# Kernel optimization log

Measured on AMD Instinct MI355X. Metric: run time of the kernel, lower is better.

## Reference

```python
import jax, jax.numpy as jnp
import numpy as np

TEMPERATURE = 30.0
LN_EPS = 1e-5

B, CIN, COUT, S, HID, K = 64, 256, 512, 4096, 64, 4


def setup_inputs() -> dict:
    key = jax.random.key(0)
    ks = jax.random.split(key, 4)
    x = jax.random.normal(ks[0], (B, CIN, S), dtype=jnp.float32)
    w1 = jax.random.normal(ks[1], (HID, CIN), dtype=jnp.float32) * (1.0 / np.sqrt(CIN))
    w2 = jax.random.normal(ks[2], (K, HID), dtype=jnp.float32) * (1.0 / np.sqrt(HID))
    b2 = jnp.zeros((K,), dtype=jnp.float32)
    conv_w = jax.random.normal(ks[3], (K, COUT, CIN), dtype=jnp.float32) * (1.0 / np.sqrt(CIN))
    conv_b = jnp.zeros((K, COUT), dtype=jnp.float32)
    gamma = jnp.ones((S,), dtype=jnp.float32)
    beta = jnp.zeros((S,), dtype=jnp.float32)
    return {"x": x, "w1": w1, "w2": w2, "b2": b2, "conv_w": conv_w,
            "conv_b": conv_b, "gamma": gamma, "beta": beta}


def reference(x, w1, w2, b2, conv_w, conv_b, gamma, beta):
    # --- attention over K kernel experts (global avg pool -> FC -> ReLU -> FC -> softmax/T) ---
    pooled = x.mean(axis=-1)                               # [B, Cin]
    h = jax.nn.relu(pooled @ w1.T)                         # [B, H]
    logits = h @ w2.T + b2                                 # [B, K]
    att = jax.nn.softmax(logits / TEMPERATURE, axis=-1)    # [B, K]
    # --- per-sample mixed 1x1 conv weights (grouped-conv trick == batched matmul) ---
    Wb = jnp.einsum('bk,koi->boi', att, conv_w)            # [B, Cout, Cin]
    bb = att @ conv_b                                      # [B, Cout]
    y = jnp.einsum('boi,bis->bos', Wb, x) + bb[:, :, None]  # [B, Cout, S]
    # --- LayerNorm over time axis (Samples) ---
    mu = y.mean(axis=-1, keepdims=True)
    var = y.var(axis=-1, keepdims=True)
    y = (y - mu) * jax.lax.rsqrt(var + LN_EPS) * gamma + beta
    # --- GELU (torch default: exact erf); dropout is identity in eval mode ---
    return jax.nn.gelu(y, approximate=False)
```

## Files before the change

### kernel.cpp

```cpp
#include <hip/hip_runtime.h>
#include <hip/hip_bf16.h>

#define B_   64
#define CIN  256
#define COUT 512
#define S_   4096
#define HID  64
#define KEXP 4

typedef float f32x4 __attribute__((ext_vector_type(4)));
typedef short bf16x8 __attribute__((ext_vector_type(8)));

static __device__ __forceinline__ unsigned short f2bf(float f) {
    union { float f; unsigned u; } c; c.f = f;
    unsigned r = c.u + 0x7FFFu + ((c.u >> 16) & 1u);
    return (unsigned short)(r >> 16);
}
static __device__ __forceinline__ float bf2f(unsigned short u) {
    union { unsigned u; float f; } c; c.u = ((unsigned)u) << 16;
    return c.f;
}

#define GSTR 68
__global__ __launch_bounds__(512, 2) void k_gram_part(const float* __restrict__ x,
                                                      float* __restrict__ part,
                                                      float* __restrict__ ppart,
                                                      unsigned short* __restrict__ xF) {
    __shared__ unsigned short lds[256 * GSTR];
    int bid = blockIdx.x;
    int b = bid & 63, sc = bid >> 6;
    int t = threadIdx.x, lane = t & 63, wv = t >> 6;
    int wr = wv >> 1, wc = wv & 1;
    const float* xb = x + (size_t)b * CIN * S_;
    unsigned short* xFb = xF + (size_t)b * S_ * CIN;

    f32x4 acc[4][8] = {};
    float psum[8] = {0.f, 0.f, 0.f, 0.f, 0.f, 0.f, 0.f, 0.f};

    for (int step = 0; step < 16; ++step) {
        int s0 = sc * 1024 + step * 64;
        __syncthreads();
#pragma unroll
        for (int p = 0; p < 8; ++p) {
            int i = t + p * 512;
            int row = i >> 4, f4 = i & 15;
            float4 v = *(const float4*)(xb + (size_t)row * S_ + s0 + f4 * 4);
            psum[p] += v.x + v.y + v.z + v.w;
            unsigned short u[4] = {f2bf(v.x), f2bf(v.y), f2bf(v.z), f2bf(v.w)};
            *(uint2*)&lds[row * GSTR + f4 * 4] = *(const uint2*)u;
        }
        __syncthreads();
        {
#pragma unroll
            for (int it = 0; it < 4; ++it) {
                int slot = t + it * 512;
                int chunk = slot >> 6;
                int st_l = chunk >> 3, kb = chunk & 7;
                int l = slot & 63;
                unsigned short tmp[8];
#pragma unroll
                for (int j = 0; j < 8; ++j)
                    tmp[j] = lds[(kb * 32 + (l >> 4) * 8 + j) * GSTR + st_l * 16 + (l & 15)];
                *(uint4*)(xFb + ((size_t)((s0 >> 4) + st_l) * 8 + kb) * 512 + l * 8) = *(const uint4*)tmp;
            }
        }
#pragma unroll
        for (int kk = 0; kk < 2; ++kk) {
            bf16x8 bfr[8];
#pragma unroll
            for (int nf = 0; nf < 8; ++nf)
                bfr[nf] = *(const bf16x8*)&lds[(wc * 128 + nf * 16 + (lane & 15)) * GSTR + kk * 32 + (lane >> 4) * 8];
#pragma unroll
            for (int mfi = 0; mfi < 4; ++mfi) {
                bf16x8 afr = *(const bf16x8*)&lds[(wr * 64 + mfi * 16 + (lane & 15)) * GSTR + kk * 32 + (lane >> 4) * 8];
#pragma unroll
                for (int nf = 0; nf < 8; ++nf)
                    acc[mfi][nf] = __builtin_amdgcn_mfma_f32_16x16x32_bf16(afr, bfr[nf], acc[mfi][nf], 0, 0, 0);
            }
        }
    }
#pragma unroll
    for (int p = 0; p < 8; ++p) {
        float s = psum[p];
        s += __shfl_xor(s, 1); s += __shfl_xor(s, 2);
        s += __shfl_xor(s, 4); s += __shfl_xor(s, 8);
        if ((t & 15) == 0) ppart[((size_t)sc * 64 + b) * 256 + ((t + p * 512) >> 4)] = s;
    }
    float* pb = part + ((size_t)sc * 64 + b) * 65536;
#pragma unroll
    for (int mfi = 0; mfi < 4; ++mfi) {
#pragma unroll
        for (int r = 0; r < 4; ++r) {
            int row = wr * 64 + mfi * 16 + (lane >> 4) * 4 + r;
#pragma unroll
            for (int nf = 0; nf < 8; ++nf)
                pb[row * 256 + wc * 128 + nf * 16 + (lane & 15)] = acc[mfi][nf][r];
        }
    }
}

__global__ __launch_bounds__(256) void k_gred(const float* __restrict__ part,
                                              const float* __restrict__ ppart,
                                              unsigned short* __restrict__ ghat,
                                              float* __restrict__ pooled) {
    int b = blockIdx.x, t = threadIdx.x;
    const size_t bo = (size_t)b * 65536;
    const size_t scs = (size_t)64 * 65536;
    const float inv = 1.f / S_;
    for (int it = 0; it < 64; ++it) {
        size_t i = (size_t)(it * 256 + t) * 4;
        float4 a0 = *(const float4*)(part + bo + i);
        float4 a1 = *(const float4*)(part + scs + bo + i);
        float4 a2 = *(const float4*)(part + 2 * scs + bo + i);
        float4 a3 = *(const float4*)(part + 3 * scs + bo + i);
        unsigned short u[4] = {f2bf((a0.x + a1.x + a2.x + a3.x) * inv),
                               f2bf((a0.y + a1.y + a2.y + a3.y) * inv),
                               f2bf((a0.z + a1.z + a2.z + a3.z) * inv),
                               f2bf((a0.w + a1.w + a2.w + a3.w) * inv)};
        *(uint2*)&ghat[bo + i] = *(const uint2*)u;
    }
    float p = ppart[(size_t)b * 256 + t] + ppart[(size_t)(64 + b) * 256 + t]
            + ppart[(size_t)(128 + b) * 256 + t] + ppart[(size_t)(192 + b) * 256 + t];
    pooled[b * 256 + t] = p * inv;
}

__global__ __launch_bounds__(64) void k_att(const float* __restrict__ pooled,
                                            const float* __restrict__ w1,
                                            const float* __restrict__ w2,
                                            const float* __restrict__ b2,
                                            float* __restrict__ att_out) {
    int b = blockIdx.x, t = threadIdx.x;
    __shared__ float pl[CIN];
    __shared__ float hl[HID];
    __shared__ float satt[KEXP];
    for (int j = t; j < CIN; j += 64) pl[j] = pooled[b * CIN + j];
    __syncthreads();
    float acc = 0.f;
    const float* w1r = w1 + t * CIN;
#pragma unroll 4
    for (int c = 0; c < CIN; c += 4) {
        float4 w = *(const float4*)(w1r + c);
        acc += w.x * pl[c] + w.y * pl[c + 1] + w.z * pl[c + 2] + w.w * pl[c + 3];
    }
    hl[t] = fmaxf(acc, 0.f);
    __syncthreads();
    if (t < KEXP) {
        float a = 0.f;
        for (int j = 0; j < HID; ++j) a += hl[j] * w2[t * HID + j];
        satt[t] = (a + b2[t]) * (1.0f / 30.0f);
    }
    __syncthreads();
    if (t == 0) {
        float m = fmaxf(fmaxf(satt[0], satt[1]), fmaxf(satt[2], satt[3]));
        float e0 = expf(satt[0] - m), e1 = expf(satt[1] - m);
        float e2 = expf(satt[2] - m), e3 = expf(satt[3] - m);
        float inv = 1.f / (e0 + e1 + e2 + e3);
        att_out[b * KEXP + 0] = e0 * inv;
        att_out[b * KEXP + 1] = e1 * inv;
        att_out[b * KEXP + 2] = e2 * inv;
        att_out[b * KEXP + 3] = e3 * inv;
    }
}

__global__ __launch_bounds__(256) void k_wb(const float* __restrict__ conv_w,
                                            const float* __restrict__ att,
                                            unsigned short* __restrict__ wb) {
    int bid = blockIdx.x;
    int b = bid >> 5, o0 = (bid & 31) * 16;
    int t = threadIdx.x;
    int o = o0 + (t >> 4);
    int i0 = (t & 15) * 16;
    float ak[KEXP];
#pragma unroll
    for (int k = 0; k < KEXP; ++k) ak[k] = att[b * KEXP + k];
    float acc[16];
#pragma unroll
    for (int j = 0; j < 16; ++j) acc[j] = 0.f;
#pragma unroll
    for (int k = 0; k < KEXP; ++k) {
        const float* src = conv_w + ((size_t)(k * COUT + o)) * CIN + i0;
#pragma unroll
        for (int j4 = 0; j4 < 4; ++j4) {
            float4 v = *(const float4*)(src + j4 * 4);
            acc[j4 * 4 + 0] += ak[k] * v.x;
            acc[j4 * 4 + 1] += ak[k] * v.y;
            acc[j4 * 4 + 2] += ak[k] * v.z;
            acc[j4 * 4 + 3] += ak[k] * v.w;
        }
    }
    unsigned short us[16];
#pragma unroll
    for (int j = 0; j < 16; ++j) us[j] = f2bf(acc[j]);
    unsigned short* dst = wb + (size_t)(b * COUT + o) * CIN + i0;
    *(uint4*)(dst) = *(const uint4*)(us);
    *(uint4*)(dst + 8) = *(const uint4*)(us + 8);
}

#define ASTR 264

__global__ __launch_bounds__(256, 2) void k_z(const unsigned short* __restrict__ wb,
                                              const unsigned short* __restrict__ ghat,
                                              float* __restrict__ zout) {
    __shared__ unsigned short lds_a[128 * ASTR];
    int bid = blockIdx.x;
    int b = bid & 63;
    int tile = bid >> 6;
    int m0 = (tile & 3) * 128, n0 = (tile >> 2) * 128;
    int t = threadIdx.x;
    {
        int row = t >> 1, half = t & 1;
        const unsigned short* src = wb + (size_t)(b * COUT + m0 + row) * CIN + half * 128;
        unsigned short* dstrow = &lds_a[row * ASTR + half * 128];
#pragma unroll
        for (int j = 0; j < 16; ++j)
            *(uint4*)(dstrow + j * 8) = *(const uint4*)(src + j * 8);
    }
    __syncthreads();

    int lane = t & 63;
    int wid = t >> 6;
    int arow = lane & 15;
    int kq = lane >> 4;
    int col0 = n0 + wid * 32 + (lane & 15);
    int col1 = col0 + 16;
    const unsigned short* gb = ghat + (size_t)b * 256 * 256;

    f32x4 acc[8][2] = {};
#pragma unroll
    for (int kk = 0; kk < 8; ++kk) {
        bf16x8 b0 = *(const bf16x8*)(gb + (size_t)col0 * 256 + kk * 32 + kq * 8);
        bf16x8 b1 = *(const bf16x8*)(gb + (size_t)col1 * 256 + kk * 32 + kq * 8);
#pragma unroll
        for (int mf = 0; mf < 8; ++mf) {
            int row = mf * 16 + arow;
            bf16x8 a = *(const bf16x8*)&lds_a[row * ASTR + kk * 32 + kq * 8];
            acc[mf][0] = __builtin_amdgcn_mfma_f32_16x16x32_bf16(a, b0, acc[mf][0], 0, 0, 0);
            acc[mf][1] = __builtin_amdgcn_mfma_f32_16x16x32_bf16(a, b1, acc[mf][1], 0, 0, 0);
        }
    }
#pragma unroll
    for (int mf = 0; mf < 8; ++mf) {
#pragma unroll
        for (int r = 0; r < 4; ++r) {
            int row = m0 + mf * 16 + (lane >> 4) * 4 + r;
            size_t rb = ((size_t)b * COUT + row) * 256;
#pragma unroll
            for (int nf = 0; nf < 2; ++nf) {
                int col = n0 + wid * 32 + nf * 16 + (lane & 15);
                zout[rb + col] = acc[mf][nf][r];
            }
        }
    }
}

__global__ __launch_bounds__(256) void k_v(const float* __restrict__ z,
                                           const unsigned short* __restrict__ wb,
                                           const float* __restrict__ pooled,
                                           float* __restrict__ mu,
                                           float* __restrict__ rstd) {
    int gid = blockIdx.x * 4 + (threadIdx.x >> 6);
    int lane = threadIdx.x & 63;
    int b = gid >> 9;
    const float* zr = z + (size_t)gid * 256;
    const unsigned short* wr = wb + (size_t)gid * 256;

    float4 zv = *(const float4*)(zr + lane * 4);
    ushort4 wu = *(const ushort4*)(wr + lane * 4);
    float w0 = bf2f(wu.x), w1 = bf2f(wu.y), w2 = bf2f(wu.z), w3 = bf2f(wu.w);
    float4 pv = *(const float4*)(pooled + b * CIN + lane * 4);

    float v = zv.x * w0 + zv.y * w1 + zv.z * w2 + zv.w * w3;
    float m = pv.x * w0 + pv.y * w1 + pv.z * w2 + pv.w * w3;
#pragma unroll
    for (int off = 1; off < 64; off <<= 1) {
        v += __shfl_xor(v, off);
        m += __shfl_xor(m, off);
    }
    if (lane == 0) {
        float var = v - m * m;
        mu[gid] = m;
        rstd[gid] = rsqrtf(var + 1e-5f);
    }
}

__global__ __launch_bounds__(512, 1) void k_main5(const unsigned short* __restrict__ xF,
                                                  const unsigned short* __restrict__ wb,
                                                  const float* __restrict__ mu,
                                                  const float* __restrict__ rstd,
                                                  const float* __restrict__ gamma,
                                                  const float* __restrict__ beta,
                                                  float* __restrict__ out) {
    __shared__ unsigned short lds_a[256 * 256];
    __shared__ unsigned short bbuf[8192];

    int bid = blockIdx.x;
    int batch = (bid & 7) * 8 + ((bid >> 3) & 7);
    int m0 = ((bid >> 6) & 1) * 256;
    int sh = (bid >> 7) & 1;

    int t = threadIdx.x, lane = t & 63;
    int w = t >> 6;
    int mgrp = w & 3, cb = w >> 2;
    int lm = lane & 15, lk = lane >> 4;

    const unsigned short* wbb = wb + (size_t)(batch * COUT + m0) * CIN;
#pragma unroll
    for (int it = 0; it < 16; ++it) {
        int i = it * 512 + t;
        int chunk = i >> 6, l = i & 63;
        int row = (chunk >> 3) * 16 + (l & 15);
        int kk = chunk & 7;
        uint4 v = *(const uint4*)(wbb + (size_t)row * CIN + kk * 32 + (l >> 4) * 8);
        *(uint4*)&lds_a[(size_t)i * 8] = v;
    }

    float mu_r[16], rs_r[16];
#pragma unroll
    for (int mf = 0; mf < 4; ++mf)
#pragma unroll
        for (int rr = 0; rr < 4; ++rr) {
            int row = batch * COUT + m0 + mgrp * 64 + mf * 16 + lk * 4 + rr;
            mu_r[mf * 4 + rr] = mu[row];
            rs_r[mf * 4 + rr] = rstd[row];
        }

    const unsigned short* xFb = xF + (size_t)batch * S_ * CIN;
    {
        size_t sb = (size_t)(sh * 128) * 4096;
        uint4 a = *(const uint4*)(xFb + sb + (size_t)t * 8);
        uint4 b = *(const uint4*)(xFb + sb + (size_t)(512 + t) * 8);
        *(uint4*)&bbuf[t * 8] = a;
        *(uint4*)&bbuf[(512 + t) * 8] = b;
    }
    __syncthreads();

    f32x4 acc[4] = {};
    for (int s = 0; s < 64; ++s) {
        uint4 xa, xb2;
        if (s < 63) {
            size_t sb = (size_t)(sh * 128 + (s + 1) * 2) * 4096;
            xa  = *(const uint4*)(xFb + sb + (size_t)t * 8);
            xb2 = *(const uint4*)(xFb + sb + (size_t)(512 + t) * 8);
        }
#pragma unroll
        for (int kk = 0; kk < 8; ++kk) {
            bf16x8 bfr = *(const bf16x8*)&bbuf[cb * 4096 + kk * 512 + lane * 8];
#pragma unroll
            for (int mf = 0; mf < 4; ++mf) {
                bf16x8 afr = *(const bf16x8*)&lds_a[(size_t)(((mgrp * 4 + mf) * 8 + kk) * 512) + lane * 8];
                acc[mf] = __builtin_amdgcn_mfma_f32_16x16x32_bf16(afr, bfr, acc[mf], 0, 0, 0);
            }
        }
        int col = sh * 2048 + s * 32 + cb * 16 + lm;
        float g = gamma[col], be = beta[col];
#pragma unroll
        for (int mf = 0; mf < 4; ++mf) {
#pragma unroll
            for (int rr = 0; rr < 4; ++rr) {
                float z = (acc[mf][rr] - mu_r[mf * 4 + rr]) * rs_r[mf * 4 + rr] * g + be;
                int row = m0 + mgrp * 64 + mf * 16 + lk * 4 + rr;
                out[(size_t)(batch * COUT + row) * S_ + col] =
                    0.5f * z * (1.f + erff(z * 0.70710678118f));
            }
            acc[mf] = (f32x4){0.f, 0.f, 0.f, 0.f};
        }
        __syncthreads();
        if (s < 63) {
            *(uint4*)&bbuf[t * 8] = xa;
            *(uint4*)&bbuf[(512 + t) * 8] = xb2;
        }
        __syncthreads();
    }
}

extern "C" void kernel_launch(void* const* d_in, const int* in_sizes, int n_in,
                              void* d_out, int out_size, void* d_ws, size_t ws_size,
                              hipStream_t stream) {
    const float* x      = (const float*)d_in[0];
    const float* w1     = (const float*)d_in[1];
    const float* w2     = (const float*)d_in[2];
    const float* b2     = (const float*)d_in[3];
    const float* conv_w = (const float*)d_in[4];
    const float* gamma  = (const float*)d_in[6];
    const float* beta   = (const float*)d_in[7];
    float* out = (float*)d_out;

    float* pooled = (float*)d_ws;
    float* att    = (float*)((char*)d_ws + 65536);
    unsigned short* wb   = (unsigned short*)((char*)d_ws + 262144);
    unsigned short* ghat = (unsigned short*)((char*)d_ws + 17039360);
    float* mu   = (float*)((char*)d_ws + 25427968);
    float* rstd = (float*)((char*)d_ws + 25559040);
    float* ppart = (float*)((char*)d_ws + 25690112);
    unsigned short* xF = (unsigned short*)((char*)d_ws + 33554432);

    float* part = out;
    float* zbuf = (float*)((char*)d_out + 67108864);

    k_gram_part<<<256, 512, 0, stream>>>(x, part, ppart, xF);
    k_gred<<<B_, 256, 0, stream>>>(part, ppart, ghat, pooled);
    k_att<<<B_, 64, 0, stream>>>(pooled, w1, w2, b2, att);
    k_wb<<<B_ * 32, 256, 0, stream>>>(conv_w, att, wb);
    k_z<<<512, 256, 0, stream>>>(wb, ghat, zbuf);
    k_v<<<B_ * COUT / 4, 256, 0, stream>>>(zbuf, wb, pooled, mu, rstd);
    k_main5<<<256, 512, 0, stream>>>(xF, wb, mu, rstd, gamma, beta, out);
}
```

Before: 509.0 us.

## Restructure main GEMM into register-resident A with double-buffered global B loads

The final fused GEMM+LayerNorm+GELU kernel is rewritten to use 1024 smaller blocks of 256 threads, each handling 64 output rows. The weight fragments are held in registers and the x fragments are loaded from global memory into register double buffers. This removes the LDS staging and per-step barriers for B. The exact erf GELU is replaced by a tanh-style approximation using exp and a fast reciprocal, which lowers epilogue cost at a small accuracy cost.

New measurement: 576.1 us. +13.2%, slower.

```diff
diff --git a/kernel.cpp b/kernel.cpp
--- a/kernel.cpp
+++ b/kernel.cpp
@@ -283,94 +283,83 @@
     }
 }
 
-__global__ __launch_bounds__(512, 1) void k_main5(const unsigned short* __restrict__ xF,
-                                                  const unsigned short* __restrict__ wb,
-                                                  const float* __restrict__ mu,
-                                                  const float* __restrict__ rstd,
-                                                  const float* __restrict__ gamma,
-                                                  const float* __restrict__ beta,
-                                                  float* __restrict__ out) {
-    __shared__ unsigned short lds_a[256 * 256];
-    __shared__ unsigned short bbuf[8192];
-
+static __device__ __forceinline__ void loadB(bf16x8 (&dst)[8], const unsigned short* p) {
+#pragma unroll
+    for (int kk = 0; kk < 8; ++kk) dst[kk] = *(const bf16x8*)(p + kk * 512);
+}
+
+__global__ __launch_bounds__(256) void k_main6(const unsigned short* __restrict__ xF,
+                                               const unsigned short* __restrict__ wb,
+                                               const float* __restrict__ mu,
+                                               const float* __restrict__ rstd,
+                                               const float* __restrict__ gamma,
+                                               const float* __restrict__ beta,
+                                               float* __restrict__ out) {
+    __shared__ unsigned short lds_a[64 * 256];
     int bid = blockIdx.x;
-    int batch = (bid & 7) * 8 + ((bid >> 3) & 7);
-    int m0 = ((bid >> 6) & 1) * 256;
-    int sh = (bid >> 7) & 1;
-
-    int t = threadIdx.x, lane = t & 63;
-    int w = t >> 6;
-    int mgrp = w & 3, cb = w >> 2;
+    int xcd = bid & 7;
+    int local = bid >> 3;
+    int mt = local & 7;
+    int sh = (local >> 3) & 1;
+    int bq = local >> 4;
+    int b = xcd + 8 * bq;
+    int m0 = mt * 64;
+
+    int t = threadIdx.x, lane = t & 63, w = t >> 6;
     int lm = lane & 15, lk = lane >> 4;
 
-    const unsigned short* wbb = wb + (size_t)(batch * COUT + m0) * CIN;
-#pragma unroll
-    for (int it = 0; it < 16; ++it) {
-        int i = it * 512 + t;
-        int chunk = i >> 6, l = i & 63;
-        int row = (chunk >> 3) * 16 + (l & 15);
-        int kk = chunk & 7;
-        uint4 v = *(const uint4*)(wbb + (size_t)row * CIN + kk * 32 + (l >> 4) * 8);
-        *(uint4*)&lds_a[(size_t)i * 8] = v;
-    }
-
-    float mu_r[16], rs_r[16];
-#pragma unroll
-    for (int mf = 0; mf < 4; ++mf)
-#pragma unroll
-        for (int rr = 0; rr < 4; ++rr) {
-            int row = batch * COUT + m0 + mgrp * 64 + mf * 16 + lk * 4 + rr;
-            mu_r[mf * 4 + rr] = mu[row];
-            rs_r[mf * 4 + rr] = rstd[row];
-        }
-
-    const unsigned short* xFb = xF + (size_t)batch * S_ * CIN;
-    {
-        size_t sb = (size_t)(sh * 128) * 4096;
-        uint4 a = *(const uint4*)(xFb + sb + (size_t)t * 8);
-        uint4 b = *(const uint4*)(xFb + sb + (size_t)(512 + t) * 8);
-        *(uint4*)&bbuf[t * 8] = a;
-        *(uint4*)&bbuf[(512 + t) * 8] = b;
-    }
-    __syncthreads();
-
-    f32x4 acc[4] = {};
-    for (int s = 0; s < 64; ++s) {
-        uint4 xa, xb2;
-        if (s < 63) {
-            size_t sb = (size_t)(sh * 128 + (s + 1) * 2) * 4096;
-            xa  = *(const uint4*)(xFb + sb + (size_t)t * 8);
-            xb2 = *(const uint4*)(xFb + sb + (size_t)(512 + t) * 8);
-        }
-#pragma unroll
-        for (int kk = 0; kk < 8; ++kk) {
-            bf16x8 bfr = *(const bf16x8*)&bbuf[cb * 4096 + kk * 512 + lane * 8];
-#pragma unroll
-            for (int mf = 0; mf < 4; ++mf) {
-                bf16x8 afr = *(const bf16x8*)&lds_a[(size_t)(((mgrp * 4 + mf) * 8 + kk) * 512) + lane * 8];
-                acc[mf] = __builtin_amdgcn_mfma_f32_16x16x32_bf16(afr, bfr, acc[mf], 0, 0, 0);
-            }
-        }
-        int col = sh * 2048 + s * 32 + cb * 16 + lm;
-        float g = gamma[col], be = beta[col];
-#pragma unroll
-        for (int mf = 0; mf < 4; ++mf) {
-#pragma unroll
-            for (int rr = 0; rr < 4; ++rr) {
-                float z = (acc[mf][rr] - mu_r[mf * 4 + rr]) * rs_r[mf * 4 + rr] * g + be;
-                int row = m0 + mgrp * 64 + mf * 16 + lk * 4 + rr;
-                out[(size_t)(batch * COUT + row) * S_ + col] =
-                    0.5f * z * (1.f + erff(z * 0.70710678118f));
-            }
-            acc[mf] = (f32x4){0.f, 0.f, 0.f, 0.f};
-        }
-        __syncthreads();
-        if (s < 63) {
-            *(uint4*)&bbuf[t * 8] = xa;
-            *(uint4*)&bbuf[(512 + t) * 8] = xb2;
-        }
-        __syncthreads();
-    }
+    const unsigned short* wbb = wb + (size_t)(b * COUT + m0) * CIN;
+#pragma unroll
+    for (int it = 0; it < 8; ++it) {
+        int i = it * 256 + t;
+        *(uint4*)&lds_a[i * 8] = *(const uint4*)(wbb + (size_t)i * 8);
+    }
+    __syncthreads();
+    bf16x8 A[8];
+#pragma unroll
+    for (int kk = 0; kk < 8; ++kk)
+        A[kk] = *(const bf16x8*)&lds_a[(w * 16 + lm) * 256 + kk * 32 + lk * 8];
+
+    float mu_r[4], rs_r[4];
+    size_t rowb[4];
+#pragma unroll
+    for (int rr = 0; rr < 4; ++rr) {
+        int row = b * COUT + m0 + w * 16 + lk * 4 + rr;
+        mu_r[rr] = mu[row];
+        rs_r[rr] = rstd[row];
+        rowb[rr] = (size_t)row * S_;
+    }
+
+    const unsigned short* xFb = xF + (size_t)b * S_ * CIN + (size_t)(sh * 128) * 4096 + lane * 8;
+    const int scb = sh * 2048;
+
+    bf16x8 B0[8], B1[8];
+    loadB(B0, xFb);
+
+#define STEP(st_, Bc)                                                              \
+    {                                                                              \
+        f32x4 a0 = {0.f, 0.f, 0.f, 0.f}, a1 = {0.f, 0.f, 0.f, 0.f};               \
+        _Pragma("unroll") for (int kk = 0; kk < 4; ++kk) {                         \
+            a0 = __builtin_amdgcn_mfma_f32_16x16x32_bf16(A[2 * kk], Bc[2 * kk], a0, 0, 0, 0);       \
+            a1 = __builtin_amdgcn_mfma_f32_16x16x32_bf16(A[2 * kk + 1], Bc[2 * kk + 1], a1, 0, 0, 0); \
+        }                                                                          \
+        int col = scb + (st_) * 16 + lm;                                           \
+        float g = gamma[col], be = beta[col];                                      \
+        _Pragma("unroll") for (int rr = 0; rr < 4; ++rr) {                         \
+            float z = (a0[rr] + a1[rr] - mu_r[rr]) * rs_r[rr] * g + be;            \
+            float d = -1.5957691216f * z * (1.f + 0.044715f * z * z);              \
+            out[rowb[rr] + col] = z * __builtin_amdgcn_rcpf(1.f + __expf(d));      \
+        }                                                                          \
+    }
+
+    for (int st = 0; st < 128; st += 2) {
+        int s2 = (st + 2 < 127) ? st + 2 : 127;
+        loadB(B1, xFb + (size_t)(st + 1) * 4096);
+        STEP(st, B0)
+        loadB(B0, xFb + (size_t)s2 * 4096);
+        STEP(st + 1, B1)
+    }
+#undef STEP
 }
 
 extern "C" void kernel_launch(void* const* d_in, const int* in_sizes, int n_in,
@@ -403,5 +392,5 @@
     k_wb<<<B_ * 32, 256, 0, stream>>>(conv_w, att, wb);
     k_z<<<512, 256, 0, stream>>>(wb, ghat, zbuf);
     k_v<<<B_ * COUT / 4, 256, 0, stream>>>(zbuf, wb, pooled, mu, rstd);
-    k_main5<<<256, 512, 0, stream>>>(xF, wb, mu, rstd, gamma, beta, out);
-}
+    k_main6<<<1024, 256, 0, stream>>>(xF, wb, mu, rstd, gamma, beta, out);
+}
```
